# Performance work log

Hardware: AMD Instinct MI355X
Metric: run time of the kernel (lower is better)

The kernel has to match this reference:

```python
import jax, jax.numpy as jnp
import numpy as np

B, L, A = 512, 2048, 3  # batch, seq_len, num_atoms


def _batched_tmscore(pred, true, coord_mask, mask):
    """Batched masked Kabsch alignment + TM-score.

    pred, true: [B, L, A, 3] coordinates
    coord_mask: [B, L, A] bool (valid atoms)
    mask:       [B, L] bool (valid residues; sum gives n for d0 formula)
    returns:    [B] TM-score per sample
    """
    Bn = pred.shape[0]
    P = pred.reshape(Bn, -1, 3)   # [B, N, 3], N = L*A
    Q = true.reshape(Bn, -1, 3)
    w = coord_mask.reshape(Bn, -1).astype(pred.dtype)  # [B, N] binary weights
    cnt = jnp.sum(w, axis=-1)                          # [B] number of valid points
    cs = jnp.maximum(cnt, 1.0)[:, None, None]

    # masked centroids
    muP = jnp.sum(w[..., None] * P, axis=1, keepdims=True) / cs
    muQ = jnp.sum(w[..., None] * Q, axis=1, keepdims=True) / cs
    # center and zero-out invalid points (w is binary so w^2 == w)
    Pc = (P - muP) * w[..., None]
    Qc = (Q - muQ) * w[..., None]

    # cross-covariance [B, 3, 3] and batched SVD-based Kabsch rotation
    H = jnp.einsum('bni,bnj->bij', Pc, Qc)
    U, S, Vt = jnp.linalg.svd(H)
    det = jnp.sign(jnp.linalg.det(U) * jnp.linalg.det(Vt))  # reflection fix
    V = jnp.swapaxes(Vt, -1, -2)
    e = jnp.stack([jnp.ones_like(det), jnp.ones_like(det), det], axis=-1)  # [B,3]
    R = jnp.einsum('bik,bjk->bij', V * e[:, None, :], U)  # R = V diag(1,1,d) U^T

    # rotate pred onto true: aligned_j = R[j,i] * Pc_i
    aligned = jnp.einsum('bji,bni->bnj', R, Pc)
    dist2 = jnp.sum((aligned - Qc) ** 2, axis=-1)  # [B, N]; 0 at masked-out points

    # TM-score: d0 = 1.24*(n-15)^(1/3) - 1.8 with n = residue count
    n = jnp.sum(mask.astype(pred.dtype), axis=-1)  # [B]
    d0 = 1.24 * jnp.cbrt(jnp.maximum(n - 15.0, 1e-3)) - 1.8
    d0 = jnp.maximum(d0, 1e-3)
    tm_terms = 1.0 / (1.0 + dist2 / (d0 ** 2)[:, None])
    tm = jnp.sum(w * tm_terms, axis=-1) / jnp.maximum(cnt, 1.0)
    return jnp.where(cnt > 0, tm, 0.0)


def setup_inputs() -> dict:
    key = jax.random.key(0)
    k1, k2, k3, k4 = jax.random.split(key, 4)
    pred_points = jax.random.normal(k1, (B, L, A, 3), dtype=jnp.float32) * 10.0
    true_points = jax.random.normal(k2, (B, L, A, 3), dtype=jnp.float32) * 10.0
    mask = jax.random.bernoulli(k3, 0.9, (B, L))
    coord_mask = mask[..., None] & jax.random.bernoulli(k4, 0.95, (B, L, A))
    return {"pred_points": pred_points, "true_points": true_points,
            "coord_mask": coord_mask, "mask": mask}


def reference(pred_points, true_points, coord_mask, mask):
    return _batched_tmscore(pred_points, true_points, coord_mask, mask)
```

## Files before the change

kernel.cpp:

```cpp
#include <hip/hip_runtime.h>
#include <math.h>

#define BATCH 512
#define SEQL  2048
#define NPTS  (SEQL*3)
#define NFLT  (NPTS*3)
#define NGRP  (NPTS/4)
#define TPB   512
#define NWAVE (TPB/64)
#define STASH 768

__device__ __forceinline__ int detect_flag(const void* cm, int* slds) {
    unsigned int v = ((const unsigned int*)cm)[threadIdx.x & 255];
    bool vi = (v <= 1u);
    bool vb = ((v & 0xFEFEFEFEu) == 0u);
    bool wi = __all(vi);
    bool wb = __all(vb);
    int wid = threadIdx.x >> 6;
    if ((threadIdx.x & 63) == 0) slds[wid] = (wi ? 1 : 0) | (wb ? 2 : 0);
    __syncthreads();
    if (threadIdx.x == 0) {
        int m = 3;
        for (int w = 0; w < (int)(blockDim.x >> 6); ++w) m &= slds[w];
        slds[8] = (m & 1) ? 0 : ((m & 2) ? 1 : 2);
    }
    __syncthreads();
    return slds[8];
}

__device__ __forceinline__ void load_mask4(const void* m, int flag, size_t g, float* w) {
    if (flag == 1) {
        unsigned int v = ((const unsigned int*)m)[g];
        w[0] = (v & 0x000000FFu) ? 1.f : 0.f;
        w[1] = (v & 0x0000FF00u) ? 1.f : 0.f;
        w[2] = (v & 0x00FF0000u) ? 1.f : 0.f;
        w[3] = (v & 0xFF000000u) ? 1.f : 0.f;
    } else if (flag == 0) {
        int4 v = ((const int4*)m)[g];
        w[0] = v.x ? 1.f : 0.f; w[1] = v.y ? 1.f : 0.f;
        w[2] = v.z ? 1.f : 0.f; w[3] = v.w ? 1.f : 0.f;
    } else {
        float4 v = ((const float4*)m)[g];
        w[0] = v.x != 0.f ? 1.f : 0.f; w[1] = v.y != 0.f ? 1.f : 0.f;
        w[2] = v.z != 0.f ? 1.f : 0.f; w[3] = v.w != 0.f ? 1.f : 0.f;
    }
}

template <int K>
__device__ __forceinline__ void block_reduce(float* acc, float* lds) {
#pragma unroll
    for (int k = 0; k < K; ++k) {
#pragma unroll
        for (int off = 32; off > 0; off >>= 1)
            acc[k] += __shfl_down(acc[k], off, 64);
    }
    int lane = threadIdx.x & 63;
    int wid  = threadIdx.x >> 6;
    if (lane == 0) {
#pragma unroll
        for (int k = 0; k < K; ++k) lds[wid * K + k] = acc[k];
    }
    __syncthreads();
    if (threadIdx.x == 0) {
#pragma unroll
        for (int k = 0; k < K; ++k) {
            float s = 0.f;
#pragma unroll
            for (int w = 0; w < NWAVE; ++w) s += lds[w * K + k];
            acc[k] = s;
        }
    }
}

__device__ __forceinline__ void accum_pt(float* a, float w,
                                         float px, float py, float pz,
                                         float qx, float qy, float qz) {
    a[0] += w;
    float wpx = w * px, wpy = w * py, wpz = w * pz;
    a[1] += wpx; a[2] += wpy; a[3] += wpz;
    a[4] += w * qx; a[5] += w * qy; a[6] += w * qz;
    a[7]  += wpx * qx; a[8]  += wpx * qy; a[9]  += wpx * qz;
    a[10] += wpy * qx; a[11] += wpy * qy; a[12] += wpy * qz;
    a[13] += wpz * qx; a[14] += wpz * qy; a[15] += wpz * qz;
}

__device__ void kabsch_params(const float* s, float* o) {
    double cnt = (double)s[0];
    double cs = fmax(cnt, 1.0);
    double mup0 = (double)s[1] / cs, mup1 = (double)s[2] / cs, mup2 = (double)s[3] / cs;
    double muq0 = (double)s[4] / cs, muq1 = (double)s[5] / cs, muq2 = (double)s[6] / cs;

    double h00 = (double)s[7]  - cnt * mup0 * muq0;
    double h01 = (double)s[8]  - cnt * mup0 * muq1;
    double h02 = (double)s[9]  - cnt * mup0 * muq2;
    double h10 = (double)s[10] - cnt * mup1 * muq0;
    double h11 = (double)s[11] - cnt * mup1 * muq1;
    double h12 = (double)s[12] - cnt * mup1 * muq2;
    double h20 = (double)s[13] - cnt * mup2 * muq0;
    double h21 = (double)s[14] - cnt * mup2 * muq1;
    double h22 = (double)s[15] - cnt * mup2 * muq2;

    double a00 = h00*h00 + h10*h10 + h20*h20;
    double a01 = h00*h01 + h10*h11 + h20*h21;
    double a02 = h00*h02 + h10*h12 + h20*h22;
    double a11 = h01*h01 + h11*h11 + h21*h21;
    double a12 = h01*h02 + h11*h12 + h21*h22;
    double a22 = h02*h02 + h12*h12 + h22*h22;

    double q3  = (a00 + a11 + a22) / 3.0;
    double pp1 = a01*a01 + a02*a02 + a12*a12;
    double b00 = a00 - q3, b11 = a11 - q3, b22 = a22 - q3;
    double pp2 = b00*b00 + b11*b11 + b22*b22 + 2.0 * pp1;

    double l0, l1, l2;
    double v1x, v1y, v1z, v2x, v2y, v2z, v3x, v3y, v3z;
    if (pp2 <= 1e-24 * (q3 * q3) + 1e-290) {
        l0 = l1 = l2 = q3;
        v1x = 1; v1y = 0; v1z = 0;
        v2x = 0; v2y = 1; v2z = 0;
        v3x = 0; v3y = 0; v3z = 1;
    } else {
        double p = sqrt(pp2 / 6.0), invp = 1.0 / p;
        double c00 = b00*invp, c01 = a01*invp, c02 = a02*invp;
        double c11 = b11*invp, c12 = a12*invp, c22 = b22*invp;
        double detB = c00*(c11*c22 - c12*c12) - c01*(c01*c22 - c12*c02)
                    + c02*(c01*c12 - c11*c02);
        double r = fmin(1.0, fmax(-1.0, detB * 0.5));
        double phi = acos(r) / 3.0;
        l0 = q3 + 2.0 * p * cos(phi);
        l2 = q3 + 2.0 * p * cos(phi + 2.0943951023931953);
        l1 = 3.0 * q3 - l0 - l2;

        double aa00 = a00*a00 + a01*a01 + a02*a02;
        double aa01 = a00*a01 + a01*a11 + a02*a12;
        double aa02 = a00*a02 + a01*a12 + a02*a22;
        double aa11 = a01*a01 + a11*a11 + a12*a12;
        double aa12 = a01*a02 + a11*a12 + a12*a22;
        double aa22 = a02*a02 + a12*a12 + a22*a22;

        double s12 = l1 + l2, p12 = l1 * l2;
        double m00 = aa00 - s12*a00 + p12;
        double m01 = aa01 - s12*a01;
        double m02 = aa02 - s12*a02;
        double m11 = aa11 - s12*a11 + p12;
        double m12 = aa12 - s12*a12;
        double m22 = aa22 - s12*a22 + p12;
        double n0 = m00*m00 + m01*m01 + m02*m02;
        double n1 = m01*m01 + m11*m11 + m12*m12;
        double n2 = m02*m02 + m12*m12 + m22*m22;
        bool s0 = (n0 >= n1) && (n0 >= n2);
        bool sA = (n1 >= n2);
        v1x = s0 ? m00 : (sA ? m01 : m02);
        v1y = s0 ? m01 : (sA ? m11 : m12);
        v1z = s0 ? m02 : (sA ? m12 : m22);
        double n1v = sqrt(v1x*v1x + v1y*v1y + v1z*v1z);
        if (n1v > 1e-150) { v1x /= n1v; v1y /= n1v; v1z /= n1v; }
        else { v1x = 1; v1y = 0; v1z = 0; }

        double s01 = l0 + l1, p01 = l0 * l1;
        double t00 = aa00 - s01*a00 + p01;
        double t01 = aa01 - s01*a01;
        double t02 = aa02 - s01*a02;
        double t11 = aa11 - s01*a11 + p01;
        double t12 = aa12 - s01*a12;
        double t22 = aa22 - s01*a22 + p01;
        double u0n = t00*t00 + t01*t01 + t02*t02;
        double u1n = t01*t01 + t11*t11 + t12*t12;
        double u2n = t02*t02 + t12*t12 + t22*t22;
        bool d0c = (u0n >= u1n) && (u0n >= u2n);
        bool dA = (u1n >= u2n);
        v3x = d0c ? t00 : (dA ? t01 : t02);
        v3y = d0c ? t01 : (dA ? t11 : t12);
        v3z = d0c ? t02 : (dA ? t12 : t22);
        double dot13 = v3x*v1x + v3y*v1y + v3z*v1z;
        v3x -= dot13 * v1x; v3y -= dot13 * v1y; v3z -= dot13 * v1z;
        double n3v = sqrt(v3x*v3x + v3y*v3y + v3z*v3z);
        if (n3v > 1e-150) { v3x /= n3v; v3y /= n3v; v3z /= n3v; }
        else {
            double A0 = fabs(v1x), A1 = fabs(v1y), A2 = fabs(v1z);
            double axx = 0, axy = 0, axz = 0;
            if (A0 <= A1 && A0 <= A2) axx = 1; else if (A1 <= A2) axy = 1; else axz = 1;
            double dd = axx*v1x + axy*v1y + axz*v1z;
            v3x = axx - dd*v1x; v3y = axy - dd*v1y; v3z = axz - dd*v1z;
            double nn = sqrt(v3x*v3x + v3y*v3y + v3z*v3z);
            v3x /= nn; v3y /= nn; v3z /= nn;
        }
        v2x = v3y*v1z - v3z*v1y;
        v2y = v3z*v1x - v3x*v1z;
        v2z = v3x*v1y - v3y*v1x;
    }

    double sv0 = sqrt(fmax(l0, 0.0));
    double sv1 = sqrt(fmax(l1, 0.0));
    double sv2 = sqrt(fmax(l2, 0.0));
    double eps = sv0 * 1e-12 + 1e-300;

    double u0x, u0y, u0z, u1x, u1y, u1z, u2x, u2y, u2z;
    {
        double hx = h00*v1x + h01*v1y + h02*v1z;
        double hy = h10*v1x + h11*v1y + h12*v1z;
        double hz = h20*v1x + h21*v1y + h22*v1z;
        if (sv0 > eps) {
            double ix = hx / sv0, iy = hy / sv0, iz = hz / sv0;
            double nn = sqrt(ix*ix + iy*iy + iz*iz);
            if (nn > 1e-300) { ix /= nn; iy /= nn; iz /= nn; }
            u0x = ix; u0y = iy; u0z = iz;
        } else { u0x = 1; u0y = 0; u0z = 0; }
    }
    {
        double hx = h00*v2x + h01*v2y + h02*v2z;
        double hy = h10*v2x + h11*v2y + h12*v2z;
        double hz = h20*v2x + h21*v2y + h22*v2z;
        if (sv1 > eps) {
            double ix = hx / sv1, iy = hy / sv1, iz = hz / sv1;
            double nn = sqrt(ix*ix + iy*iy + iz*iz);
            if (nn > 1e-300) { ix /= nn; iy /= nn; iz /= nn; }
            u1x = ix; u1y = iy; u1z = iz;
        } else {
            double A0 = fabs(u0x), A1 = fabs(u0y), A2 = fabs(u0z);
            double axx = 0, axy = 0, axz = 0;
            if (A0 <= A1 && A0 <= A2) axx = 1; else if (A1 <= A2) axy = 1; else axz = 1;
            double cx = u0y*axz - u0z*axy;
            double cy = u0z*axx - u0x*axz;
            double cz = u0x*axy - u0y*axx;
            double nn = sqrt(cx*cx + cy*cy + cz*cz);
            if (nn > 1e-300) { cx /= nn; cy /= nn; cz /= nn; }
            u1x = cx; u1y = cy; u1z = cz;
        }
    }
    {
        double hx = h00*v3x + h01*v3y + h02*v3z;
        double hy = h10*v3x + h11*v3y + h12*v3z;
        double hz = h20*v3x + h21*v3y + h22*v3z;
        if (sv2 > eps) {
            double ix = hx / sv2, iy = hy / sv2, iz = hz / sv2;
            double nn = sqrt(ix*ix + iy*iy + iz*iz);
            if (nn > 1e-300) { ix /= nn; iy /= nn; iz /= nn; }
            u2x = ix; u2y = iy; u2z = iz;
        } else {
            u2x = u0y*u1z - u0z*u1y;
            u2y = u0z*u1x - u0x*u1z;
            u2z = u0x*u1y - u0y*u1x;
            double nn = sqrt(u2x*u2x + u2y*u2y + u2z*u2z);
            if (nn > 1e-300) { u2x /= nn; u2y /= nn; u2z /= nn; }
        }
    }

    double detH = h00*(h11*h22 - h12*h21) - h01*(h10*h22 - h12*h20)
                + h02*(h10*h21 - h11*h20);
    double e2 = (detH > 0.0) ? 1.0 : ((detH < 0.0) ? -1.0 : 0.0);

    o[0] = (float)(v1x*u0x + v2x*u1x + e2*v3x*u2x);
    o[1] = (float)(v1x*u0y + v2x*u1y + e2*v3x*u2y);
    o[2] = (float)(v1x*u0z + v2x*u1z + e2*v3x*u2z);
    o[3] = (float)(v1y*u0x + v2y*u1x + e2*v3y*u2x);
    o[4] = (float)(v1y*u0y + v2y*u1y + e2*v3y*u2y);
    o[5] = (float)(v1y*u0z + v2y*u1z + e2*v3y*u2z);
    o[6] = (float)(v1z*u0x + v2z*u1x + e2*v3z*u2x);
    o[7] = (float)(v1z*u0y + v2z*u1y + e2*v3z*u2y);
    o[8] = (float)(v1z*u0z + v2z*u1z + e2*v3z*u2z);

    double n = (double)s[16];
    double d0 = 1.24 * cbrt(fmax(n - 15.0, 1e-3)) - 1.8;
    d0 = fmax(d0, 1e-3);
    o[9]  = (float)mup0; o[10] = (float)mup1; o[11] = (float)mup2;
    o[12] = (float)muq0; o[13] = (float)muq1; o[14] = (float)muq2;
    o[15] = (float)(1.0 / (d0 * d0));
    o[16] = (float)cnt;
}

__global__ __launch_bounds__(TPB, 4) void k_fused(
    const float* __restrict__ P, const float* __restrict__ Q,
    const void* __restrict__ cmask, const void* __restrict__ rmask,
    float* __restrict__ out) {
    int b = blockIdx.x;
    __shared__ int slds[9];
    __shared__ float lds[NWAVE * 17];
    __shared__ float prm[17];
    __shared__ float4 sP0[STASH], sP1[STASH], sP2[STASH];
    __shared__ float4 sQ0[STASH], sQ1[STASH], sQ2[STASH];
    int flag = detect_flag(cmask, slds);

    const float4* Pv = (const float4*)(P + (size_t)b * NFLT);
    const float4* Qv = (const float4*)(Q + (size_t)b * NFLT);
    size_t gbase = (size_t)b * NGRP;

    float acc[17];
#pragma unroll
    for (int k = 0; k < 17; ++k) acc[k] = 0.0f;

    {
        size_t rg = (size_t)b * (SEQL / 4) + threadIdx.x;
        if (flag == 1) {
            unsigned int v = ((const unsigned int*)rmask)[rg];
            acc[16] = (float)__popc(v);
        } else if (flag == 0) {
            int4 v = ((const int4*)rmask)[rg];
            acc[16] = (v.x ? 1.f : 0.f) + (v.y ? 1.f : 0.f) + (v.z ? 1.f : 0.f) + (v.w ? 1.f : 0.f);
        } else {
            float4 v = ((const float4*)rmask)[rg];
            acc[16] = (v.x != 0.f ? 1.f : 0.f) + (v.y != 0.f ? 1.f : 0.f)
                    + (v.z != 0.f ? 1.f : 0.f) + (v.w != 0.f ? 1.f : 0.f);
        }
    }

#pragma unroll
    for (int it = 0; it < 3; ++it) {
        int g = threadIdx.x + it * TPB;
        float4 p0 = Pv[3 * g + 0], p1 = Pv[3 * g + 1], p2 = Pv[3 * g + 2];
        float4 q0 = Qv[3 * g + 0], q1 = Qv[3 * g + 1], q2 = Qv[3 * g + 2];
        float w[4];
        load_mask4(cmask, flag, gbase + g, w);
        if (g < STASH) {
            sP0[g] = p0; sP1[g] = p1; sP2[g] = p2;
            sQ0[g] = q0; sQ1[g] = q1; sQ2[g] = q2;
        }
        accum_pt(acc, w[0], p0.x, p0.y, p0.z, q0.x, q0.y, q0.z);
        accum_pt(acc, w[1], p0.w, p1.x, p1.y, q0.w, q1.x, q1.y);
        accum_pt(acc, w[2], p1.z, p1.w, p2.x, q1.z, q1.w, q2.x);
        accum_pt(acc, w[3], p2.y, p2.z, p2.w, q2.y, q2.z, q2.w);
    }

    block_reduce<17>(acc, lds);

    if (threadIdx.x == 0) kabsch_params(acc, prm);
    __syncthreads();

    float R0 = prm[0], R1 = prm[1], R2 = prm[2];
    float R3 = prm[3], R4 = prm[4], R5 = prm[5];
    float R6 = prm[6], R7 = prm[7], R8 = prm[8];
    float mpx = prm[9], mpy = prm[10], mpz = prm[11];
    float mqx = prm[12], mqy = prm[13], mqz = prm[14];
    float inv = prm[15], cnt = prm[16];

    float acc2[1] = {0.0f};
#pragma unroll
    for (int it = 0; it < 3; ++it) {
        int g = threadIdx.x + it * TPB;
        float4 p0, p1, p2, q0, q1, q2;
        if (g < STASH) {
            p0 = sP0[g]; p1 = sP1[g]; p2 = sP2[g];
            q0 = sQ0[g]; q1 = sQ1[g]; q2 = sQ2[g];
        } else {
            p0 = Pv[3 * g + 0]; p1 = Pv[3 * g + 1]; p2 = Pv[3 * g + 2];
            q0 = Qv[3 * g + 0]; q1 = Qv[3 * g + 1]; q2 = Qv[3 * g + 2];
        }
        float w[4];
        load_mask4(cmask, flag, gbase + g, w);
        float px[4] = {p0.x, p0.w, p1.z, p2.y};
        float py[4] = {p0.y, p1.x, p1.w, p2.z};
        float pz[4] = {p0.z, p1.y, p2.x, p2.w};
        float qx[4] = {q0.x, q0.w, q1.z, q2.y};
        float qy[4] = {q0.y, q1.x, q1.w, q2.z};
        float qz[4] = {q0.z, q1.y, q2.x, q2.w};
#pragma unroll
        for (int u = 0; u < 4; ++u) {
            float pcx = px[u] - mpx, pcy = py[u] - mpy, pcz = pz[u] - mpz;
            float ax = R0 * pcx + R1 * pcy + R2 * pcz;
            float ay = R3 * pcx + R4 * pcy + R5 * pcz;
            float az = R6 * pcx + R7 * pcy + R8 * pcz;
            float dx = ax - (qx[u] - mqx);
            float dy = ay - (qy[u] - mqy);
            float dz = az - (qz[u] - mqz);
            float d2 = dx * dx + dy * dy + dz * dz;
            acc2[0] += w[u] / (1.0f + d2 * inv);
        }
    }
    __syncthreads();
    block_reduce<1>(acc2, lds);
    if (threadIdx.x == 0)
        out[b] = (cnt > 0.0f) ? acc2[0] / fmaxf(cnt, 1.0f) : 0.0f;
}

extern "C" void kernel_launch(void* const* d_in, const int* in_sizes, int n_in,
                              void* d_out, int out_size, void* d_ws, size_t ws_size,
                              hipStream_t stream) {
    const float* P = (const float*)d_in[0];
    const float* Q = (const float*)d_in[1];
    const void* cm = d_in[2];
    const void* rm = d_in[3];
    float* out = (float*)d_out;

    k_fused<<<BATCH, TPB, 0, stream>>>(P, Q, cm, rm, out);
}
```

Before: 33.38 us.

## Hoist all loads up front, keep masks in registers, prefetch pass-2 reloads, fold centroids into translation

Pass 1 now issues all P/Q and mask loads at the start, before any arithmetic. The mask weights stay in registers, so pass 2 no longer reloads them. The non-stashed P/Q data that pass 2 must re-fetch from global memory is now requested before the pass-2 math, so its latency overlaps the LDS reads. Separately, the two centroids are folded into one precomputed translation vector, which saves subtractions per point. The costs are higher register pressure, which may reduce occupancy, and a slightly different float rounding order.

```diff
diff --git a/kernel.cpp b/kernel.cpp
--- a/kernel.cpp
+++ b/kernel.cpp
@@ -250,23 +250,29 @@
                 + h02*(h10*h21 - h11*h20);
     double e2 = (detH > 0.0) ? 1.0 : ((detH < 0.0) ? -1.0 : 0.0);
 
-    o[0] = (float)(v1x*u0x + v2x*u1x + e2*v3x*u2x);
-    o[1] = (float)(v1x*u0y + v2x*u1y + e2*v3x*u2y);
-    o[2] = (float)(v1x*u0z + v2x*u1z + e2*v3x*u2z);
-    o[3] = (float)(v1y*u0x + v2y*u1x + e2*v3y*u2x);
-    o[4] = (float)(v1y*u0y + v2y*u1y + e2*v3y*u2y);
-    o[5] = (float)(v1y*u0z + v2y*u1z + e2*v3y*u2z);
-    o[6] = (float)(v1z*u0x + v2z*u1x + e2*v3z*u2x);
-    o[7] = (float)(v1z*u0y + v2z*u1y + e2*v3z*u2y);
-    o[8] = (float)(v1z*u0z + v2z*u1z + e2*v3z*u2z);
+    double R00 = v1x*u0x + v2x*u1x + e2*v3x*u2x;
+    double R01 = v1x*u0y + v2x*u1y + e2*v3x*u2y;
+    double R02 = v1x*u0z + v2x*u1z + e2*v3x*u2z;
+    double R10 = v1y*u0x + v2y*u1x + e2*v3y*u2x;
+    double R11 = v1y*u0y + v2y*u1y + e2*v3y*u2y;
+    double R12 = v1y*u0z + v2y*u1z + e2*v3y*u2z;
+    double R20 = v1z*u0x + v2z*u1x + e2*v3z*u2x;
+    double R21 = v1z*u0y + v2z*u1y + e2*v3z*u2y;
+    double R22 = v1z*u0z + v2z*u1z + e2*v3z*u2z;
+
+    o[0] = (float)R00; o[1] = (float)R01; o[2] = (float)R02;
+    o[3] = (float)R10; o[4] = (float)R11; o[5] = (float)R12;
+    o[6] = (float)R20; o[7] = (float)R21; o[8] = (float)R22;
+
+    o[9]  = (float)(R00*mup0 + R01*mup1 + R02*mup2 - muq0);
+    o[10] = (float)(R10*mup0 + R11*mup1 + R12*mup2 - muq1);
+    o[11] = (float)(R20*mup0 + R21*mup1 + R22*mup2 - muq2);
 
     double n = (double)s[16];
     double d0 = 1.24 * cbrt(fmax(n - 15.0, 1e-3)) - 1.8;
     d0 = fmax(d0, 1e-3);
-    o[9]  = (float)mup0; o[10] = (float)mup1; o[11] = (float)mup2;
-    o[12] = (float)muq0; o[13] = (float)muq1; o[14] = (float)muq2;
-    o[15] = (float)(1.0 / (d0 * d0));
-    o[16] = (float)cnt;
+    o[12] = (float)(1.0 / (d0 * d0));
+    o[13] = (float)cnt;
 }
 
 __global__ __launch_bounds__(TPB, 4) void k_fused(
@@ -274,9 +280,10 @@
     const void* __restrict__ cmask, const void* __restrict__ rmask,
     float* __restrict__ out) {
     int b = blockIdx.x;
+    int tid = threadIdx.x;
     __shared__ int slds[9];
     __shared__ float lds[NWAVE * 17];
-    __shared__ float prm[17];
+    __shared__ float prm[14];
     __shared__ float4 sP0[STASH], sP1[STASH], sP2[STASH];
     __shared__ float4 sQ0[STASH], sQ1[STASH], sQ2[STASH];
     int flag = detect_flag(cmask, slds);
@@ -285,68 +292,113 @@
     const float4* Qv = (const float4*)(Q + (size_t)b * NFLT);
     size_t gbase = (size_t)b * NGRP;
 
+    float4 p[9], q[9];
+#pragma unroll
+    for (int k = 0; k < 3; ++k) {
+        int g = tid + k * TPB;
+        p[3*k+0] = Pv[3*g+0]; p[3*k+1] = Pv[3*g+1]; p[3*k+2] = Pv[3*g+2];
+        q[3*k+0] = Qv[3*g+0]; q[3*k+1] = Qv[3*g+1]; q[3*k+2] = Qv[3*g+2];
+    }
+    float w[12];
+    float rescnt;
+    {
+        size_t rg = (size_t)b * (SEQL / 4) + tid;
+        if (flag == 0) {
+            const int4* cm4 = (const int4*)cmask;
+            int4 m0 = cm4[gbase + tid], m1 = cm4[gbase + tid + TPB], m2 = cm4[gbase + tid + 2*TPB];
+            int4 rv = ((const int4*)rmask)[rg];
+            w[0]=m0.x?1.f:0.f; w[1]=m0.y?1.f:0.f; w[2]=m0.z?1.f:0.f; w[3]=m0.w?1.f:0.f;
+            w[4]=m1.x?1.f:0.f; w[5]=m1.y?1.f:0.f; w[6]=m1.z?1.f:0.f; w[7]=m1.w?1.f:0.f;
+            w[8]=m2.x?1.f:0.f; w[9]=m2.y?1.f:0.f; w[10]=m2.z?1.f:0.f; w[11]=m2.w?1.f:0.f;
+            rescnt = (rv.x?1.f:0.f) + (rv.y?1.f:0.f) + (rv.z?1.f:0.f) + (rv.w?1.f:0.f);
+        } else if (flag == 1) {
+            const unsigned int* cmw = (const unsigned int*)cmask;
+            unsigned int m0 = cmw[gbase + tid], m1 = cmw[gbase + tid + TPB], m2 = cmw[gbase + tid + 2*TPB];
+            unsigned int rv = ((const unsigned int*)rmask)[rg];
+            w[0]=(m0&0xFFu)?1.f:0.f; w[1]=(m0&0xFF00u)?1.f:0.f; w[2]=(m0&0xFF0000u)?1.f:0.f; w[3]=(m0&0xFF000000u)?1.f:0.f;
+            w[4]=(m1&0xFFu)?1.f:0.f; w[5]=(m1&0xFF00u)?1.f:0.f; w[6]=(m1&0xFF0000u)?1.f:0.f; w[7]=(m1&0xFF000000u)?1.f:0.f;
+            w[8]=(m2&0xFFu)?1.f:0.f; w[9]=(m2&0xFF00u)?1.f:0.f; w[10]=(m2&0xFF0000u)?1.f:0.f; w[11]=(m2&0xFF000000u)?1.f:0.f;
+            rescnt = (float)__popc(rv);
+        } else {
+            const float4* cmf = (const float4*)cmask;
+            float4 m0 = cmf[gbase + tid], m1 = cmf[gbase + tid + TPB], m2 = cmf[gbase + tid + 2*TPB];
+            float4 rv = ((const float4*)rmask)[rg];
+            w[0]=m0.x!=0.f?1.f:0.f; w[1]=m0.y!=0.f?1.f:0.f; w[2]=m0.z!=0.f?1.f:0.f; w[3]=m0.w!=0.f?1.f:0.f;
+            w[4]=m1.x!=0.f?1.f:0.f; w[5]=m1.y!=0.f?1.f:0.f; w[6]=m1.z!=0.f?1.f:0.f; w[7]=m1.w!=0.f?1.f:0.f;
+            w[8]=m2.x!=0.f?1.f:0.f; w[9]=m2.y!=0.f?1.f:0.f; w[10]=m2.z!=0.f?1.f:0.f; w[11]=m2.w!=0.f?1.f:0.f;
+            rescnt = (rv.x!=0.f?1.f:0.f) + (rv.y!=0.f?1.f:0.f) + (rv.z!=0.f?1.f:0.f) + (rv.w!=0.f?1.f:0.f);
+        }
+    }
+
+#pragma unroll
+    for (int k = 0; k < 3; ++k) {
+        int g = tid + k * TPB;
+        if (g < STASH) {
+            sP0[g] = p[3*k+0]; sP1[g] = p[3*k+1]; sP2[g] = p[3*k+2];
+            sQ0[g] = q[3*k+0]; sQ1[g] = q[3*k+1]; sQ2[g] = q[3*k+2];
+        }
+    }
+
     float acc[17];
 #pragma unroll
     for (int k = 0; k < 17; ++k) acc[k] = 0.0f;
-
-    {
-        size_t rg = (size_t)b * (SEQL / 4) + threadIdx.x;
-        if (flag == 1) {
-            unsigned int v = ((const unsigned int*)rmask)[rg];
-            acc[16] = (float)__popc(v);
-        } else if (flag == 0) {
-            int4 v = ((const int4*)rmask)[rg];
-            acc[16] = (v.x ? 1.f : 0.f) + (v.y ? 1.f : 0.f) + (v.z ? 1.f : 0.f) + (v.w ? 1.f : 0.f);
-        } else {
-            float4 v = ((const float4*)rmask)[rg];
-            acc[16] = (v.x != 0.f ? 1.f : 0.f) + (v.y != 0.f ? 1.f : 0.f)
-                    + (v.z != 0.f ? 1.f : 0.f) + (v.w != 0.f ? 1.f : 0.f);
-        }
-    }
-
-#pragma unroll
-    for (int it = 0; it < 3; ++it) {
-        int g = threadIdx.x + it * TPB;
-        float4 p0 = Pv[3 * g + 0], p1 = Pv[3 * g + 1], p2 = Pv[3 * g + 2];
-        float4 q0 = Qv[3 * g + 0], q1 = Qv[3 * g + 1], q2 = Qv[3 * g + 2];
-        float w[4];
-        load_mask4(cmask, flag, gbase + g, w);
-        if (g < STASH) {
-            sP0[g] = p0; sP1[g] = p1; sP2[g] = p2;
-            sQ0[g] = q0; sQ1[g] = q1; sQ2[g] = q2;
-        }
-        accum_pt(acc, w[0], p0.x, p0.y, p0.z, q0.x, q0.y, q0.z);
-        accum_pt(acc, w[1], p0.w, p1.x, p1.y, q0.w, q1.x, q1.y);
-        accum_pt(acc, w[2], p1.z, p1.w, p2.x, q1.z, q1.w, q2.x);
-        accum_pt(acc, w[3], p2.y, p2.z, p2.w, q2.y, q2.z, q2.w);
+    acc[16] = rescnt;
+
+#pragma unroll
+    for (int k = 0; k < 3; ++k) {
+        float4 p0 = p[3*k+0], p1 = p[3*k+1], p2 = p[3*k+2];
+        float4 q0 = q[3*k+0], q1 = q[3*k+1], q2 = q[3*k+2];
+        accum_pt(acc, w[4*k+0], p0.x, p0.y, p0.z, q0.x, q0.y, q0.z);
+        accum_pt(acc, w[4*k+1], p0.w, p1.x, p1.y, q0.w, q1.x, q1.y);
+        accum_pt(acc, w[4*k+2], p1.z, p1.w, p2.x, q1.z, q1.w, q2.x);
+        accum_pt(acc, w[4*k+3], p2.y, p2.z, p2.w, q2.y, q2.z, q2.w);
     }
 
     block_reduce<17>(acc, lds);
 
-    if (threadIdx.x == 0) kabsch_params(acc, prm);
+    if (tid == 0) kabsch_params(acc, prm);
     __syncthreads();
 
     float R0 = prm[0], R1 = prm[1], R2 = prm[2];
     float R3 = prm[3], R4 = prm[4], R5 = prm[5];
     float R6 = prm[6], R7 = prm[7], R8 = prm[8];
-    float mpx = prm[9], mpy = prm[10], mpz = prm[11];
-    float mqx = prm[12], mqy = prm[13], mqz = prm[14];
-    float inv = prm[15], cnt = prm[16];
-
-    float acc2[1] = {0.0f};
-#pragma unroll
-    for (int it = 0; it < 3; ++it) {
-        int g = threadIdx.x + it * TPB;
+    float tx = prm[9], ty = prm[10], tz = prm[11];
+    float inv = prm[12], cnt = prm[13];
+
+    bool lds1 = (tid < STASH - TPB);
+    float4 gp0, gp1, gp2, gq0, gq1, gq2;
+    float4 hp0, hp1, hp2, hq0, hq1, hq2;
+    {
+        int g = tid + 2 * TPB;
+        gp0 = Pv[3*g+0]; gp1 = Pv[3*g+1]; gp2 = Pv[3*g+2];
+        gq0 = Qv[3*g+0]; gq1 = Qv[3*g+1]; gq2 = Qv[3*g+2];
+    }
+    if (!lds1) {
+        int g = tid + TPB;
+        hp0 = Pv[3*g+0]; hp1 = Pv[3*g+1]; hp2 = Pv[3*g+2];
+        hq0 = Qv[3*g+0]; hq1 = Qv[3*g+1]; hq2 = Qv[3*g+2];
+    }
+
+    float acc2 = 0.0f;
+#pragma unroll
+    for (int k = 0; k < 3; ++k) {
+        int g = tid + k * TPB;
         float4 p0, p1, p2, q0, q1, q2;
-        if (g < STASH) {
+        if (k == 0) {
             p0 = sP0[g]; p1 = sP1[g]; p2 = sP2[g];
             q0 = sQ0[g]; q1 = sQ1[g]; q2 = sQ2[g];
+        } else if (k == 1) {
+            if (lds1) {
+                p0 = sP0[g]; p1 = sP1[g]; p2 = sP2[g];
+                q0 = sQ0[g]; q1 = sQ1[g]; q2 = sQ2[g];
+            } else {
+                p0 = hp0; p1 = hp1; p2 = hp2;
+                q0 = hq0; q1 = hq1; q2 = hq2;
+            }
         } else {
-            p0 = Pv[3 * g + 0]; p1 = Pv[3 * g + 1]; p2 = Pv[3 * g + 2];
-            q0 = Qv[3 * g + 0]; q1 = Qv[3 * g + 1]; q2 = Qv[3 * g + 2];
-        }
-        float w[4];
-        load_mask4(cmask, flag, gbase + g, w);
+            p0 = gp0; p1 = gp1; p2 = gp2;
+            q0 = gq0; q1 = gq1; q2 = gq2;
+        }
         float px[4] = {p0.x, p0.w, p1.z, p2.y};
         float py[4] = {p0.y, p1.x, p1.w, p2.z};
         float pz[4] = {p0.z, p1.y, p2.x, p2.w};
@@ -355,21 +407,18 @@
         float qz[4] = {q0.z, q1.y, q2.x, q2.w};
 #pragma unroll
         for (int u = 0; u < 4; ++u) {
-            float pcx = px[u] - mpx, pcy = py[u] - mpy, pcz = pz[u] - mpz;
-            float ax = R0 * pcx + R1 * pcy + R2 * pcz;
-            float ay = R3 * pcx + R4 * pcy + R5 * pcz;
-            float az = R6 * pcx + R7 * pcy + R8 * pcz;
-            float dx = ax - (qx[u] - mqx);
-            float dy = ay - (qy[u] - mqy);
-            float dz = az - (qz[u] - mqz);
-            float d2 = dx * dx + dy * dy + dz * dz;
-            acc2[0] += w[u] / (1.0f + d2 * inv);
+            float dx = R0*px[u] + R1*py[u] + R2*pz[u] - tx - qx[u];
+            float dy = R3*px[u] + R4*py[u] + R5*pz[u] - ty - qy[u];
+            float dz = R6*px[u] + R7*py[u] + R8*pz[u] - tz - qz[u];
+            float d2 = dx*dx + dy*dy + dz*dz;
+            acc2 += w[4*k+u] / (1.0f + d2 * inv);
         }
     }
     __syncthreads();
-    block_reduce<1>(acc2, lds);
-    if (threadIdx.x == 0)
-        out[b] = (cnt > 0.0f) ? acc2[0] / fmaxf(cnt, 1.0f) : 0.0f;
+    float a2[1] = {acc2};
+    block_reduce<1>(a2, lds);
+    if (tid == 0)
+        out[b] = (cnt > 0.0f) ? a2[0] / fmaxf(cnt, 1.0f) : 0.0f;
 }
 
 extern "C" void kernel_launch(void* const* d_in, const int* in_sizes, int n_in,
```

Result: faster. 30.12 us (-9.8%).
